# Kernel tuning notes

Hardware: AMD Instinct MI355X
Metric: run time of the kernel (lower is better)

The kernel has to match this reference:

```python
import jax, jax.numpy as jnp
import numpy as np

NUM_HEADS = 12
DROP_RATIO = 0.25
LN_EPS = 1e-5


def _layernorm(x, g, b):
    m = jnp.mean(x, axis=-1, keepdims=True)
    v = jnp.var(x, axis=-1, keepdims=True)
    return (x - m) * jax.lax.rsqrt(v + LN_EPS) * g + b


def setup_inputs() -> dict:
    key = jax.random.key(0)
    ks = jax.random.split(key, 12)
    B, N, C = 16, 785, 768
    H = 4 * C
    s = 0.02
    return {
        "x": jax.random.normal(ks[0], (B, N, C), dtype=jnp.float32),
        "ln1_g": jnp.ones((C,), jnp.float32),
        "ln1_b": jnp.zeros((C,), jnp.float32),
        "w_qkv": jax.random.normal(ks[1], (C, 3 * C), jnp.float32) * s,  # qkv_bias=False
        "w_proj": jax.random.normal(ks[2], (C, C), jnp.float32) * s,
        "b_proj": jnp.zeros((C,), jnp.float32),
        "ln2_g": jnp.ones((C,), jnp.float32),
        "ln2_b": jnp.zeros((C,), jnp.float32),
        "w_fc1": jax.random.normal(ks[3], (C, H), jnp.float32) * s,
        "b_fc1": jnp.zeros((H,), jnp.float32),
        "w_fc2": jax.random.normal(ks[4], (H, C), jnp.float32) * s,
        "b_fc2": jnp.zeros((C,), jnp.float32),
    }


def _block(x, ln1_g, ln1_b, w_qkv, w_proj, b_proj, ln2_g, ln2_b,
           w_fc1, b_fc1, w_fc2, b_fc2):
    B, N, C = x.shape
    Hh = NUM_HEADS
    Dh = C // Hh
    scale = Dh ** -0.5
    target = N - int(N * DROP_RATIO)  # kept KV length (incl. CLS)

    h = _layernorm(x, ln1_g, ln1_b)
    qkv = (h @ w_qkv).reshape(B, N, 3, Hh, Dh).transpose(2, 0, 3, 1, 4)
    q, k, v = qkv[0], qkv[1], qkv[2]  # each [B, H, N, Dh]

    # 'low' branch: L2-norm token scoring on non-CLS k tokens, keep top (target-1)
    rem_k = k[:, :, 1:, :]
    rem_v = v[:, :, 1:, :]
    scores = jnp.linalg.norm(rem_k, axis=-1) / Dh  # [B, H, N-1]
    _, idx = jax.lax.top_k(scores, target - 1)
    idx = jnp.sort(idx, axis=-1)  # restore original token order
    idx_e = idx[..., None]
    new_k = jnp.concatenate(
        [k[:, :, :1, :], jnp.take_along_axis(rem_k, idx_e, axis=2)], axis=2)
    new_v = jnp.concatenate(
        [v[:, :, :1, :], jnp.take_along_axis(rem_v, idx_e, axis=2)], axis=2)

    attn = jnp.einsum('bhnd,bhmd->bhnm', q, new_k) * scale
    attn = jax.nn.softmax(attn, axis=-1)
    o = jnp.einsum('bhnm,bhmd->bhnd', attn, new_v)
    o = o.transpose(0, 2, 1, 3).reshape(B, N, C)
    o = o @ w_proj + b_proj
    x = x + o  # drop_path = 0

    h2 = _layernorm(x, ln2_g, ln2_b)
    m = jax.nn.gelu(h2 @ w_fc1 + b_fc1, approximate=False) @ w_fc2 + b_fc2
    return x + m


def reference(x, ln1_g, ln1_b, w_qkv, w_proj, b_proj, ln2_g, ln2_b,
              w_fc1, b_fc1, w_fc2, b_fc2):
    return _block(x, ln1_g, ln1_b, w_qkv, w_proj, b_proj, ln2_g, ln2_b,
                  w_fc1, b_fc1, w_fc2, b_fc2)
```

## Files before the change

### kernel.cpp

```cpp
#include <hip/hip_runtime.h>

#define B_ 16
#define NTOK 785
#define C_ 768
#define HH 12
#define DH 64
#define BHN (B_*HH)
#define KVLEN 589
#define KVPAD 640
#define MROWS (B_*NTOK)
#define HID 3072

typedef __bf16  bf16x8  __attribute__((ext_vector_type(8)));
typedef short   short4v __attribute__((ext_vector_type(4)));
typedef float   f32x4   __attribute__((ext_vector_type(4)));
typedef int     int4v   __attribute__((ext_vector_type(4)));
typedef unsigned short u16;

__device__ __forceinline__ u16 f2b(float f) {
  unsigned u = __builtin_bit_cast(unsigned, f);
  u = u + 0x7FFFu + ((u >> 16) & 1u);
  return (u16)(u >> 16);
}

#define AS1C(p) ((const __attribute__((address_space(1))) void*)(p))
#define AS3(p)  ((__attribute__((address_space(3))) void*)(p))
#define SWZ(row, g) ((row)*64 + ((((g) ^ ((row)&7))) << 3))

#define OFF_H   ((size_t)0)
#define OFF_KF  ((size_t)19292160)
#define OFF_QB  (OFF_KF + (size_t)38584320)
#define OFF_VB  (OFF_QB + (size_t)19292160)
#define OFF_KP  (OFF_VB + (size_t)19292160)
#define OFF_VP  (OFF_KP + (size_t)15728640)
#define OFF_OB  (OFF_VP + (size_t)15728640)
#define OFF_WQ  (OFF_OB + (size_t)19292160)
#define OFF_WP  (OFF_WQ + (size_t)3538944)
#define OFF_W1  (OFF_WP + (size_t)1179648)
#define OFF_W2  (OFF_W1 + (size_t)4718592)
#define OFF_SC  (OFF_W2 + (size_t)4718592)
#define OFF_IX  (OFF_SC + (size_t)602112)
#define OFF_G   OFF_KF

__global__ __launch_bounds__(256)
void transpose_cast(const float* __restrict__ w, u16* __restrict__ wt, int K, int N) {
  __shared__ float T[64][65];
  const int k0 = blockIdx.x * 64, n0 = blockIdx.y * 64;
  const int tid = threadIdx.x;
  const int cc = tid & 63, rr = tid >> 6;
#pragma unroll
  for (int i = 0; i < 16; ++i) {
    int r = rr + i * 4;
    T[r][cc] = w[(size_t)(k0 + r) * N + n0 + cc];
  }
  __syncthreads();
#pragma unroll
  for (int i = 0; i < 16; ++i) {
    int r = rr + i * 4;
    wt[(size_t)(n0 + r) * K + k0 + cc] = f2b(T[cc][r]);
  }
}

__global__ __launch_bounds__(256)
void ln_kernel(const float* __restrict__ x, const float* __restrict__ g,
               const float* __restrict__ b, u16* __restrict__ out) {
  const int row = blockIdx.x;
  const int tid = threadIdx.x;
  const float* xr = x + (size_t)row * C_;
  float v0 = xr[tid], v1 = xr[tid + 256], v2 = xr[tid + 512];
  float sum = v0 + v1 + v2;
  float sq  = v0 * v0 + v1 * v1 + v2 * v2;
#pragma unroll
  for (int o = 32; o > 0; o >>= 1) { sum += __shfl_xor(sum, o); sq += __shfl_xor(sq, o); }
  __shared__ float rs[4], rq[4];
  int w = tid >> 6;
  if ((tid & 63) == 0) { rs[w] = sum; rq[w] = sq; }
  __syncthreads();
  sum = rs[0] + rs[1] + rs[2] + rs[3];
  sq  = rq[0] + rq[1] + rq[2] + rq[3];
  float mean = sum * (1.0f / C_);
  float var  = sq * (1.0f / C_) - mean * mean;
  float rstd = rsqrtf(var + 1e-5f);
  u16* orow = out + (size_t)row * C_;
  orow[tid]       = f2b((v0 - mean) * rstd * g[tid]       + b[tid]);
  orow[tid + 256] = f2b((v1 - mean) * rstd * g[tid + 256] + b[tid + 256]);
  orow[tid + 512] = f2b((v2 - mean) * rstd * g[tid + 512] + b[tid + 512]);
}

template<int EPI>
__global__ __launch_bounds__(256, 2)
void gemm128(const u16* __restrict__ A, const u16* __restrict__ Bt,
             int M, int N, int K,
             const float* __restrict__ bias, const float* __restrict__ addsrc,
             float* __restrict__ outf, u16* __restrict__ outb,
             u16* __restrict__ qb, u16* __restrict__ kb, u16* __restrict__ vb,
             float* __restrict__ sc) {
  __shared__ u16 As[128 * 64];
  __shared__ u16 Bs[128 * 64];
  const int tid = threadIdx.x;
  const int lane = tid & 63;
  const int w = tid >> 6;
  const int wm = w >> 1, wn = w & 1;
  const int l15 = lane & 15;
  const int hi = lane >> 4;

  const int CN = (N + 127) >> 7;
  const int nwg = gridDim.x * gridDim.y;
  const int orig = blockIdx.x + blockIdx.y * gridDim.x;
  const int q = nwg >> 3, r8 = nwg & 7;
  const int xcd = orig & 7, pos = orig >> 3;
  const int wgid = (xcd < r8 ? xcd * (q + 1) : r8 * (q + 1) + (xcd - r8) * q) + pos;
  const int m0 = (wgid / CN) * 128;
  const int n0 = (wgid - (wgid / CN) * CN) * 128;

  const int srow = tid >> 3;
  const int sseg = tid & 7;

  f32x4 acc[4][4] = {};

  for (int kt = 0; kt < K; kt += 64) {
    __syncthreads();
#pragma unroll
    for (int i = 0; i < 4; ++i) {
      int row = i * 32 + srow;
      int gseg = sseg ^ (row & 7);
      int gr = m0 + row; if (gr >= M) gr = M - 1;
      int flat = i * 256 + tid;
      __builtin_amdgcn_global_load_lds(AS1C(A  + (size_t)gr * K         + kt + gseg * 8),
                                       AS3(&As[flat * 8]), 16, 0, 0);
      __builtin_amdgcn_global_load_lds(AS1C(Bt + (size_t)(n0 + row) * K + kt + gseg * 8),
                                       AS3(&Bs[flat * 8]), 16, 0, 0);
    }
    __syncthreads();
#pragma unroll
    for (int kk = 0; kk < 2; ++kk) {
      bf16x8 a[4], b[4];
#pragma unroll
      for (int mi = 0; mi < 4; ++mi)
        a[mi] = *reinterpret_cast<const bf16x8*>(&As[SWZ(wm * 64 + mi * 16 + l15, kk * 4 + hi)]);
#pragma unroll
      for (int ni = 0; ni < 4; ++ni)
        b[ni] = *reinterpret_cast<const bf16x8*>(&Bs[SWZ(wn * 64 + ni * 16 + l15, kk * 4 + hi)]);
#pragma unroll
      for (int mi = 0; mi < 4; ++mi)
#pragma unroll
        for (int ni = 0; ni < 4; ++ni)
          acc[mi][ni] = __builtin_amdgcn_mfma_f32_16x16x32_bf16(a[mi], b[ni], acc[mi][ni], 0, 0, 0);
    }
  }

#pragma unroll
  for (int mi = 0; mi < 4; ++mi) {
#pragma unroll
    for (int ni = 0; ni < 4; ++ni) {
#pragma unroll
      for (int j = 0; j < 4; ++j) {
        int r = m0 + wm * 64 + mi * 16 + hi * 4 + j;
        int c = n0 + wn * 64 + ni * 16 + l15;
        if (r < M) {
          float v = acc[mi][ni][j];
          if (EPI == 0) {
            int sec = (c >= 1536) ? 2 : (c >= 768 ? 1 : 0);
            int cm = c - sec * 768;
            int hh = cm >> 6, d = cm & 63;
            int bb = r / NTOK; int nn = r - bb * NTOK;
            size_t addr = (((size_t)(bb * HH + hh)) * NTOK + nn) * DH + d;
            if (sec == 0)      qb[addr] = f2b(v);
            else if (sec == 1) kb[addr] = f2b(v);
            else               vb[addr] = f2b(v);
          } else if (EPI == 1) {
            size_t o = (size_t)r * N + c;
            outf[o] = v + bias[c] + addsrc[o];
          } else if (EPI == 2) {
            float t = v + bias[c];
            outb[(size_t)r * N + c] = f2b(0.5f * t * (1.0f + erff(t * 0.70710678118654752f)));
          } else {
            size_t o = (size_t)r * N + c;
            outf[o] = v + bias[c] + addsrc[o];
          }
        }
      }
    }
  }

  if (EPI == 0) {
    int csec = n0 + wn * 64;
    if (csec >= 768 && csec < 1536) {
      int hh = (csec - 768) >> 6;
#pragma unroll
      for (int mi = 0; mi < 4; ++mi) {
#pragma unroll
        for (int j = 0; j < 4; ++j) {
          float ss = 0.0f;
#pragma unroll
          for (int ni = 0; ni < 4; ++ni) { float v = acc[mi][ni][j]; ss += v * v; }
          ss += __shfl_xor(ss, 1); ss += __shfl_xor(ss, 2);
          ss += __shfl_xor(ss, 4); ss += __shfl_xor(ss, 8);
          int r = m0 + wm * 64 + mi * 16 + hi * 4 + j;
          if (l15 == 0 && r < M) {
            int bb = r / NTOK, nn = r - bb * NTOK;
            if (nn >= 1)
              sc[(size_t)(bb * HH + hh) * 784 + nn - 1] = sqrtf(ss) * (1.0f / 64.0f);
          }
        }
      }
    }
  }
}

__global__ __launch_bounds__(512)
void topk_kernel(const float* __restrict__ scores, int* __restrict__ idxb) {
  const int bh = blockIdx.x;
  const int tid = threadIdx.x;
  __shared__ float ss[1024];
  __shared__ int   sid[1024];
  __shared__ int   sid2[1024];
  for (int i = tid; i < 1024; i += 512) {
    ss[i]  = (i < 784) ? scores[bh * 784 + i] : -__builtin_inff();
    sid[i] = i;
  }
  for (int k = 2; k <= 1024; k <<= 1) {
    for (int j = k >> 1; j > 0; j >>= 1) {
      __syncthreads();
      for (int i = tid; i < 1024; i += 512) {
        int ixj = i ^ j;
        if (ixj > i) {
          float s1 = ss[i], s2 = ss[ixj];
          int   i1 = sid[i], i2 = sid[ixj];
          bool keep = (s1 > s2) || (s1 == s2 && i1 < i2);
          bool doSwap = ((i & k) == 0) ? !keep : keep;
          if (doSwap) { ss[i] = s2; ss[ixj] = s1; sid[i] = i2; sid[ixj] = i1; }
        }
      }
    }
  }
  __syncthreads();
  for (int i = tid; i < 1024; i += 512)
    sid2[i] = (i < 588) ? sid[i] : 0x7FFFFFFF;
  for (int k = 2; k <= 1024; k <<= 1) {
    for (int j = k >> 1; j > 0; j >>= 1) {
      __syncthreads();
      for (int i = tid; i < 1024; i += 512) {
        int ixj = i ^ j;
        if (ixj > i) {
          int a = sid2[i], b2 = sid2[ixj];
          bool keep = (a < b2);
          bool doSwap = ((i & k) == 0) ? !keep : keep;
          if (doSwap) { sid2[i] = b2; sid2[ixj] = a; }
        }
      }
    }
  }
  __syncthreads();
  for (int i = tid; i < 588; i += 512) idxb[bh * 588 + i] = sid2[i];
}

__global__ __launch_bounds__(256)
void gather_kernel(const u16* __restrict__ kb, const u16* __restrict__ vb,
                   const int* __restrict__ idxb, u16* __restrict__ kp, u16* __restrict__ vpT) {
  __shared__ u16 T[64 * 64];
  const int bh = blockIdx.x, chunk = blockIdx.y, t = threadIdx.x;
  {
    int jl = t >> 2, d0 = (t & 3) * 16;
    int j = chunk * 64 + jl;
    int n = (j == 0) ? 0 : (j <= 588 ? idxb[bh * 588 + j - 1] + 1 : -1);
    int4v k0 = {}, k1 = {}, v0 = {}, v1 = {};
    if (n >= 0) {
      size_t src = ((size_t)bh * NTOK + n) * DH + d0;
      k0 = *reinterpret_cast<const int4v*>(&kb[src]);
      k1 = *reinterpret_cast<const int4v*>(&kb[src + 8]);
      v0 = *reinterpret_cast<const int4v*>(&vb[src]);
      v1 = *reinterpret_cast<const int4v*>(&vb[src + 8]);
    }
    size_t kdst = ((size_t)bh * KVPAD + j) * DH + d0;
    *reinterpret_cast<int4v*>(&kp[kdst])     = k0;
    *reinterpret_cast<int4v*>(&kp[kdst + 8]) = k1;
    *reinterpret_cast<int4v*>(&T[jl * 64 + d0])     = v0;
    *reinterpret_cast<int4v*>(&T[jl * 64 + d0 + 8]) = v1;
  }
  __syncthreads();
  {
    int d = t & 63, kvo = (t >> 6) * 16;
    alignas(16) u16 tmp[16];
#pragma unroll
    for (int i = 0; i < 16; ++i) tmp[i] = T[(kvo + i) * 64 + d];
    size_t dst = ((size_t)bh * 64 + d) * KVPAD + chunk * 64 + kvo;
    *reinterpret_cast<int4v*>(&vpT[dst])     = *reinterpret_cast<int4v*>(&tmp[0]);
    *reinterpret_cast<int4v*>(&vpT[dst + 8]) = *reinterpret_cast<int4v*>(&tmp[8]);
  }
}

__global__ __launch_bounds__(256)
void attn_kernel(const u16* __restrict__ qb, const u16* __restrict__ kp,
                 const u16* __restrict__ vpT, u16* __restrict__ ob) {
  __shared__ u16 Qs[64 * 64];
  __shared__ u16 Ks[64 * 64];
  __shared__ u16 VTs[64 * 64];
  const int tid = threadIdx.x;
  const int lane = tid & 63;
  const int w = tid >> 6;
  const int l15 = lane & 15;
  const int hi = lane >> 4;
  const int bh = blockIdx.x;
  const int n0 = blockIdx.y * 64;

#pragma unroll
  for (int i = 0; i < 2; ++i) {
    int flat = i * 256 + tid;
    int row = flat >> 3, g = flat & 7;
    int4v val = {};
    if (n0 + row < NTOK)
      val = *reinterpret_cast<const int4v*>(qb + ((size_t)bh * NTOK + n0 + row) * DH + g * 8);
    *reinterpret_cast<int4v*>(&Qs[SWZ(row, g)]) = val;
  }
  __syncthreads();
  bf16x8 q0 = *reinterpret_cast<const bf16x8*>(&Qs[SWZ(w * 16 + l15, hi)]);
  bf16x8 q1 = *reinterpret_cast<const bf16x8*>(&Qs[SWZ(w * 16 + l15, 4 + hi)]);

  float m_run = -__builtin_inff(), l_run = 0.0f;
  f32x4 oa[4] = {};

  for (int kvt = 0; kvt < 10; ++kvt) {
    int4v kr[2], vr[2];
#pragma unroll
    for (int i = 0; i < 2; ++i) {
      int flat = i * 256 + tid;
      int row = flat >> 3, g = flat & 7;
      kr[i] = *reinterpret_cast<const int4v*>(kp  + ((size_t)bh * KVPAD + kvt * 64 + row) * DH + g * 8);
      vr[i] = *reinterpret_cast<const int4v*>(vpT + ((size_t)bh * 64 + row) * KVPAD + kvt * 64 + g * 8);
    }
    __syncthreads();
#pragma unroll
    for (int i = 0; i < 2; ++i) {
      int flat = i * 256 + tid;
      int row = flat >> 3, g = flat & 7;
      *reinterpret_cast<int4v*>(&Ks[SWZ(row, g)])  = kr[i];
      *reinterpret_cast<int4v*>(&VTs[SWZ(row, g)]) = vr[i];
    }
    __syncthreads();

    f32x4 st[4];
#pragma unroll
    for (int ft = 0; ft < 4; ++ft) {
      bf16x8 a0 = *reinterpret_cast<const bf16x8*>(&Ks[SWZ(ft * 16 + l15, hi)]);
      bf16x8 a1 = *reinterpret_cast<const bf16x8*>(&Ks[SWZ(ft * 16 + l15, 4 + hi)]);
      f32x4 cfr = {};
      cfr = __builtin_amdgcn_mfma_f32_16x16x32_bf16(a0, q0, cfr, 0, 0, 0);
      cfr = __builtin_amdgcn_mfma_f32_16x16x32_bf16(a1, q1, cfr, 0, 0, 0);
      st[ft] = cfr;
    }
    float mx = -__builtin_inff();
#pragma unroll
    for (int ft = 0; ft < 4; ++ft) {
#pragma unroll
      for (int j = 0; j < 4; ++j) {
        int kv = kvt * 64 + ft * 16 + hi * 4 + j;
        float s = st[ft][j] * 0.125f;
        s = (kv < KVLEN) ? s : -__builtin_inff();
        st[ft][j] = s;
        mx = fmaxf(mx, s);
      }
    }
    mx = fmaxf(mx, __shfl_xor(mx, 16));
    mx = fmaxf(mx, __shfl_xor(mx, 32));
    float m_new = fmaxf(m_run, mx);
    float alpha = __expf(m_run - m_new);
    float psum = 0.0f;
    short4v pb[4];
#pragma unroll
    for (int ft = 0; ft < 4; ++ft) {
#pragma unroll
      for (int j = 0; j < 4; ++j) {
        float p = __expf(st[ft][j] - m_new);
        psum += p;
        pb[ft][j] = (short)f2b(p);
      }
    }
    psum += __shfl_xor(psum, 16);
    psum += __shfl_xor(psum, 32);
    l_run = l_run * alpha + psum;
    m_run = m_new;
#pragma unroll
    for (int df = 0; df < 4; ++df) {
      oa[df][0] *= alpha; oa[df][1] *= alpha; oa[df][2] *= alpha; oa[df][3] *= alpha;
    }
#pragma unroll
    for (int df = 0; df < 4; ++df) {
#pragma unroll
      for (int ft = 0; ft < 4; ++ft) {
        short4v va = *reinterpret_cast<const short4v*>(
            &VTs[SWZ(df * 16 + l15, ft * 2 + (hi >> 1)) + (hi & 1) * 4]);
        oa[df] = __builtin_amdgcn_mfma_f32_16x16x16bf16_1k(va, pb[ft], oa[df], 0, 0, 0);
      }
    }
  }
  int n = n0 + w * 16 + l15;
  if (n < NTOK) {
    float inv = 1.0f / l_run;
    int bb = bh / HH, hh = bh - bb * HH;
    size_t base = ((size_t)bb * NTOK + n) * C_ + hh * DH;
#pragma unroll
    for (int df = 0; df < 4; ++df) {
      short4v pv;
#pragma unroll
      for (int j = 0; j < 4; ++j) pv[j] = (short)f2b(oa[df][j] * inv);
      *reinterpret_cast<short4v*>(ob + base + df * 16 + hi * 4) = pv;
    }
  }
}

extern "C" void kernel_launch(void* const* d_in, const int* in_sizes, int n_in,
                              void* d_out, int out_size, void* d_ws, size_t ws_size,
                              hipStream_t stream) {
  const float* x     = (const float*)d_in[0];
  const float* ln1g  = (const float*)d_in[1];
  const float* ln1b  = (const float*)d_in[2];
  const float* wqkv  = (const float*)d_in[3];
  const float* wproj = (const float*)d_in[4];
  const float* bproj = (const float*)d_in[5];
  const float* ln2g  = (const float*)d_in[6];
  const float* ln2b  = (const float*)d_in[7];
  const float* wfc1  = (const float*)d_in[8];
  const float* bfc1  = (const float*)d_in[9];
  const float* wfc2  = (const float*)d_in[10];
  const float* bfc2  = (const float*)d_in[11];
  float* out = (float*)d_out;
  char* wsb = (char*)d_ws;

  u16*   h     = (u16*)(wsb + OFF_H);
  u16*   kb    = (u16*)(wsb + OFF_KF);
  u16*   qb    = (u16*)(wsb + OFF_QB);
  u16*   vb    = (u16*)(wsb + OFF_VB);
  u16*   kp    = (u16*)(wsb + OFF_KP);
  u16*   vpT   = (u16*)(wsb + OFF_VP);
  u16*   ob    = (u16*)(wsb + OFF_OB);
  u16*   wqT   = (u16*)(wsb + OFF_WQ);
  u16*   wpT   = (u16*)(wsb + OFF_WP);
  u16*   w1T   = (u16*)(wsb + OFF_W1);
  u16*   w2T   = (u16*)(wsb + OFF_W2);
  float* sc    = (float*)(wsb + OFF_SC);
  int*   idxb  = (int*)(wsb + OFF_IX);
  u16*   g     = (u16*)(wsb + OFF_G);

  transpose_cast<<<dim3(768 / 64, 2304 / 64), 256, 0, stream>>>(wqkv, wqT, 768, 2304);
  transpose_cast<<<dim3(768 / 64, 768 / 64),  256, 0, stream>>>(wproj, wpT, 768, 768);
  transpose_cast<<<dim3(768 / 64, 3072 / 64), 256, 0, stream>>>(wfc1, w1T, 768, 3072);
  transpose_cast<<<dim3(3072 / 64, 768 / 64), 256, 0, stream>>>(wfc2, w2T, 3072, 768);

  ln_kernel<<<MROWS, 256, 0, stream>>>(x, ln1g, ln1b, h);

  gemm128<0><<<dim3(2304 / 128, 99), 256, 0, stream>>>(h, wqT, MROWS, 2304, 768,
      nullptr, nullptr, nullptr, nullptr, qb, kb, vb, sc);

  topk_kernel<<<BHN, 512, 0, stream>>>(sc, idxb);
  gather_kernel<<<dim3(BHN, KVPAD / 64), 256, 0, stream>>>(kb, vb, idxb, kp, vpT);

  attn_kernel<<<dim3(BHN, 13), 256, 0, stream>>>(qb, kp, vpT, ob);

  gemm128<1><<<dim3(768 / 128, 99), 256, 0, stream>>>(ob, wpT, MROWS, 768, 768,
      bproj, x, out, nullptr, nullptr, nullptr, nullptr, nullptr);

  ln_kernel<<<MROWS, 256, 0, stream>>>(out, ln2g, ln2b, h);

  gemm128<2><<<dim3(3072 / 128, 99), 256, 0, stream>>>(h, w1T, MROWS, 3072, 768,
      bfc1, nullptr, nullptr, g, nullptr, nullptr, nullptr, nullptr);

  gemm128<3><<<dim3(768 / 128, 99), 256, 0, stream>>>(g, w2T, MROWS, 768, 3072,
      bfc2, out, out, nullptr, nullptr, nullptr, nullptr, nullptr);
}
```

Baseline: 457.5 us.

## Add double-buffered 256x256 GEMM kernel for QKV and FC1 projections

Adds a gemm256 kernel with 512 threads, 256x256 output tiles, double-buffered LDS staging through global_load_lds, and phased MFMA issue using s_setprio and barriers. The QKV and FC1 GEMMs move to it, while the proj and FC2 GEMMs stay on a slimmed gemm128 that keeps only the residual epilogue. Larger tiles should raise arithmetic intensity and overlap loads with compute on the wide-N GEMMs. The cost is 64KB of LDS per block and 128 accumulator floats per thread, which reduces occupancy, and the grid gets coarser (450 and 600 blocks).

```diff
diff --git a/kernel.cpp b/kernel.cpp
--- a/kernel.cpp
+++ b/kernel.cpp
@@ -88,13 +88,159 @@
 }
 
 template<int EPI>
+__global__ __launch_bounds__(512, 2)
+void gemm256(const u16* __restrict__ A, const u16* __restrict__ Bt,
+             int M, int N, int K,
+             const float* __restrict__ bias,
+             u16* __restrict__ outb,
+             u16* __restrict__ qb, u16* __restrict__ kb, u16* __restrict__ vb,
+             float* __restrict__ sc) {
+  __shared__ u16 As[2][256 * 64];
+  __shared__ u16 Bs[2][256 * 64];
+  const int tid = threadIdx.x;
+  const int lane = tid & 63;
+  const int wid = tid >> 6;
+  const int wr = wid >> 2, wc = wid & 3;
+  const int l15 = lane & 15;
+  const int hi = lane >> 4;
+
+  const int CN = N >> 8;
+  const int nwg = gridDim.x * gridDim.y;
+  const int orig = blockIdx.x + blockIdx.y * gridDim.x;
+  const int q = nwg >> 3, r8 = nwg & 7;
+  const int xcd = orig & 7, pos = orig >> 3;
+  const int wgid = (xcd < r8 ? xcd * (q + 1) : r8 * (q + 1) + (xcd - r8) * q) + pos;
+  const int m0 = (wgid / CN) * 256;
+  const int n0 = (wgid - (wgid / CN) * CN) * 256;
+
+  const int srow = tid >> 3;
+  const int sseg = tid & 7;
+  const u16* aptr[4]; const u16* bptr[4]; int fl16[4];
+#pragma unroll
+  for (int i = 0; i < 4; ++i) {
+    int row = i * 64 + srow;
+    int gseg = sseg ^ (row & 7);
+    int gra = m0 + row; if (gra >= M) gra = M - 1;
+    aptr[i] = A  + (size_t)gra * K        + gseg * 8;
+    bptr[i] = Bt + (size_t)(n0 + row) * K + gseg * 8;
+    fl16[i] = (i * 512 + tid) * 8;
+  }
+
+#define STAGE256(buf, kt)                                                        \
+  {                                                                              \
+    _Pragma("unroll")                                                            \
+    for (int i = 0; i < 4; ++i) {                                                \
+      __builtin_amdgcn_global_load_lds(AS1C(aptr[i] + (kt)),                     \
+                                       AS3(&As[buf][fl16[i]]), 16, 0, 0);        \
+      __builtin_amdgcn_global_load_lds(AS1C(bptr[i] + (kt)),                     \
+                                       AS3(&Bs[buf][fl16[i]]), 16, 0, 0);        \
+    }                                                                            \
+  }
+
+  f32x4 acc[8][4] = {};
+  const int NT = K >> 6;
+
+  STAGE256(0, 0);
+  STAGE256(1, 64);
+
+  for (int t = 0; t < NT; ++t) {
+    const int cur = t & 1;
+    if (t >= 1 && t + 1 < NT) STAGE256(cur ^ 1, (t + 1) * 64);
+    if (t + 1 < NT) asm volatile("s_waitcnt vmcnt(8)" ::: "memory");
+    else            asm volatile("s_waitcnt vmcnt(0)" ::: "memory");
+    __builtin_amdgcn_s_barrier();
+
+    bf16x8 b[4];
+#define PHASE256(mh, kk, LOADB)                                                  \
+    {                                                                            \
+      if (LOADB) {                                                               \
+        _Pragma("unroll")                                                        \
+        for (int ni = 0; ni < 4; ++ni)                                           \
+          b[ni] = *reinterpret_cast<const bf16x8*>(                              \
+              &Bs[cur][SWZ(wc * 64 + ni * 16 + l15, (kk) * 4 + hi)]);            \
+      }                                                                          \
+      bf16x8 a[4];                                                               \
+      _Pragma("unroll")                                                          \
+      for (int mi = 0; mi < 4; ++mi)                                             \
+        a[mi] = *reinterpret_cast<const bf16x8*>(                                \
+            &As[cur][SWZ(wr * 128 + (mh) * 64 + mi * 16 + l15, (kk) * 4 + hi)]); \
+      __builtin_amdgcn_s_setprio(1);                                             \
+      _Pragma("unroll")                                                          \
+      for (int mi = 0; mi < 4; ++mi)                                             \
+        _Pragma("unroll")                                                        \
+        for (int ni = 0; ni < 4; ++ni)                                           \
+          acc[(mh) * 4 + mi][ni] = __builtin_amdgcn_mfma_f32_16x16x32_bf16(      \
+              a[mi], b[ni], acc[(mh) * 4 + mi][ni], 0, 0, 0);                    \
+      __builtin_amdgcn_s_setprio(0);                                             \
+      __builtin_amdgcn_s_barrier();                                              \
+    }
+    PHASE256(0, 0, 1)
+    PHASE256(1, 0, 0)
+    PHASE256(0, 1, 1)
+    PHASE256(1, 1, 0)
+#undef PHASE256
+  }
+#undef STAGE256
+
+#pragma unroll
+  for (int am = 0; am < 8; ++am) {
+#pragma unroll
+    for (int ni = 0; ni < 4; ++ni) {
+#pragma unroll
+      for (int j = 0; j < 4; ++j) {
+        int r = m0 + wr * 128 + am * 16 + hi * 4 + j;
+        int c = n0 + wc * 64 + ni * 16 + l15;
+        if (r < M) {
+          float v = acc[am][ni][j];
+          if (EPI == 0) {
+            int sec = (c >= 1536) ? 2 : (c >= 768 ? 1 : 0);
+            int cm = c - sec * 768;
+            int hh = cm >> 6, d = cm & 63;
+            int bb = r / NTOK; int nn = r - bb * NTOK;
+            size_t addr = (((size_t)(bb * HH + hh)) * NTOK + nn) * DH + d;
+            if (sec == 0)      qb[addr] = f2b(v);
+            else if (sec == 1) kb[addr] = f2b(v);
+            else               vb[addr] = f2b(v);
+          } else {
+            float tt = v + bias[c];
+            outb[(size_t)r * N + c] = f2b(0.5f * tt * (1.0f + erff(tt * 0.70710678118654752f)));
+          }
+        }
+      }
+    }
+  }
+
+  if (EPI == 0) {
+    int csec = n0 + wc * 64;
+    if (csec >= 768 && csec < 1536) {
+      int hh = (csec - 768) >> 6;
+#pragma unroll
+      for (int am = 0; am < 8; ++am) {
+#pragma unroll
+        for (int j = 0; j < 4; ++j) {
+          float ss = 0.0f;
+#pragma unroll
+          for (int ni = 0; ni < 4; ++ni) { float v = acc[am][ni][j]; ss += v * v; }
+          ss += __shfl_xor(ss, 1); ss += __shfl_xor(ss, 2);
+          ss += __shfl_xor(ss, 4); ss += __shfl_xor(ss, 8);
+          int r = m0 + wr * 128 + am * 16 + hi * 4 + j;
+          if (l15 == 0 && r < M) {
+            int bb = r / NTOK, nn = r - bb * NTOK;
+            if (nn >= 1)
+              sc[(size_t)(bb * HH + hh) * 784 + nn - 1] = sqrtf(ss) * (1.0f / 64.0f);
+          }
+        }
+      }
+    }
+  }
+}
+
+template<int EPI>
 __global__ __launch_bounds__(256, 2)
 void gemm128(const u16* __restrict__ A, const u16* __restrict__ Bt,
              int M, int N, int K,
              const float* __restrict__ bias, const float* __restrict__ addsrc,
-             float* __restrict__ outf, u16* __restrict__ outb,
-             u16* __restrict__ qb, u16* __restrict__ kb, u16* __restrict__ vb,
-             float* __restrict__ sc) {
+             float* __restrict__ outf) {
   __shared__ u16 As[128 * 64];
   __shared__ u16 Bs[128 * 64];
   const int tid = threadIdx.x;
@@ -158,50 +304,8 @@
         int r = m0 + wm * 64 + mi * 16 + hi * 4 + j;
         int c = n0 + wn * 64 + ni * 16 + l15;
         if (r < M) {
-          float v = acc[mi][ni][j];
-          if (EPI == 0) {
-            int sec = (c >= 1536) ? 2 : (c >= 768 ? 1 : 0);
-            int cm = c - sec * 768;
-            int hh = cm >> 6, d = cm & 63;
-            int bb = r / NTOK; int nn = r - bb * NTOK;
-            size_t addr = (((size_t)(bb * HH + hh)) * NTOK + nn) * DH + d;
-            if (sec == 0)      qb[addr] = f2b(v);
-            else if (sec == 1) kb[addr] = f2b(v);
-            else               vb[addr] = f2b(v);
-          } else if (EPI == 1) {
-            size_t o = (size_t)r * N + c;
-            outf[o] = v + bias[c] + addsrc[o];
-          } else if (EPI == 2) {
-            float t = v + bias[c];
-            outb[(size_t)r * N + c] = f2b(0.5f * t * (1.0f + erff(t * 0.70710678118654752f)));
-          } else {
-            size_t o = (size_t)r * N + c;
-            outf[o] = v + bias[c] + addsrc[o];
-          }
-        }
-      }
-    }
-  }
-
-  if (EPI == 0) {
-    int csec = n0 + wn * 64;
-    if (csec >= 768 && csec < 1536) {
-      int hh = (csec - 768) >> 6;
-#pragma unroll
-      for (int mi = 0; mi < 4; ++mi) {
-#pragma unroll
-        for (int j = 0; j < 4; ++j) {
-          float ss = 0.0f;
-#pragma unroll
-          for (int ni = 0; ni < 4; ++ni) { float v = acc[mi][ni][j]; ss += v * v; }
-          ss += __shfl_xor(ss, 1); ss += __shfl_xor(ss, 2);
-          ss += __shfl_xor(ss, 4); ss += __shfl_xor(ss, 8);
-          int r = m0 + wm * 64 + mi * 16 + hi * 4 + j;
-          if (l15 == 0 && r < M) {
-            int bb = r / NTOK, nn = r - bb * NTOK;
-            if (nn >= 1)
-              sc[(size_t)(bb * HH + hh) * 784 + nn - 1] = sqrtf(ss) * (1.0f / 64.0f);
-          }
+          size_t o = (size_t)r * N + c;
+          outf[o] = acc[mi][ni][j] + bias[c] + addsrc[o];
         }
       }
     }
@@ -449,8 +553,8 @@
 
   ln_kernel<<<MROWS, 256, 0, stream>>>(x, ln1g, ln1b, h);
 
-  gemm128<0><<<dim3(2304 / 128, 99), 256, 0, stream>>>(h, wqT, MROWS, 2304, 768,
-      nullptr, nullptr, nullptr, nullptr, qb, kb, vb, sc);
+  gemm256<0><<<dim3(2304 / 256, 50), 512, 0, stream>>>(h, wqT, MROWS, 2304, 768,
+      nullptr, nullptr, qb, kb, vb, sc);
 
   topk_kernel<<<BHN, 512, 0, stream>>>(sc, idxb);
   gather_kernel<<<dim3(BHN, KVPAD / 64), 256, 0, stream>>>(kb, vb, idxb, kp, vpT);
@@ -458,13 +562,13 @@
   attn_kernel<<<dim3(BHN, 13), 256, 0, stream>>>(qb, kp, vpT, ob);
 
   gemm128<1><<<dim3(768 / 128, 99), 256, 0, stream>>>(ob, wpT, MROWS, 768, 768,
-      bproj, x, out, nullptr, nullptr, nullptr, nullptr, nullptr);
+      bproj, x, out);
 
   ln_kernel<<<MROWS, 256, 0, stream>>>(out, ln2g, ln2b, h);
 
-  gemm128<2><<<dim3(3072 / 128, 99), 256, 0, stream>>>(h, w1T, MROWS, 3072, 768,
-      bfc1, nullptr, nullptr, g, nullptr, nullptr, nullptr, nullptr);
+  gemm256<2><<<dim3(3072 / 256, 50), 512, 0, stream>>>(h, w1T, MROWS, 3072, 768,
+      bfc1, g, nullptr, nullptr, nullptr, nullptr);
 
   gemm128<3><<<dim3(768 / 128, 99), 256, 0, stream>>>(g, w2T, MROWS, 768, 3072,
-      bfc2, out, out, nullptr, nullptr, nullptr, nullptr, nullptr);
-}
+      bfc2, out, out);
+}
```

Result: slower. 524.6 us (+14.7%).
